# Kernel optimization log

Measured on AMD Instinct MI355X. Metric: run time of the kernel, lower is better.

The kernel has to match this reference:

```python
import jax, jax.numpy as jnp
import numpy as np

E = 1024   # embedding_dim
A = 1024   # attention_dim
H = 16     # num_heads
D = A // H # head_dim


def setup_inputs() -> dict:
    key = jax.random.key(0)
    ks = jax.random.split(key, 9)
    s = 1.0 / np.sqrt(E)
    so = 1.0 / np.sqrt(A)
    return {
        "x": jax.random.normal(ks[0], (2, 2048, E), dtype=jnp.float32),
        "Wq": jax.random.uniform(ks[1], (E, A), jnp.float32, -s, s),
        "bq": jax.random.uniform(ks[2], (A,), jnp.float32, -s, s),
        "Wk": jax.random.uniform(ks[3], (E, A), jnp.float32, -s, s),
        "bk": jax.random.uniform(ks[4], (A,), jnp.float32, -s, s),
        "Wv": jax.random.uniform(ks[5], (E, A), jnp.float32, -s, s),
        "bv": jax.random.uniform(ks[6], (A,), jnp.float32, -s, s),
        "Wo": jax.random.uniform(ks[7], (A, E), jnp.float32, -so, so),
        "bo": jax.random.uniform(ks[8], (E,), jnp.float32, -so, so),
    }


def reference(x, Wq, bq, Wk, bk, Wv, bv, Wo, bo):
    B, S, _ = x.shape
    # projections -> [B, H, S, D]
    def split_heads(t):
        return t.reshape(B, S, H, D).transpose(0, 2, 1, 3)
    Q = split_heads(x @ Wq + bq)
    K = split_heads(x @ Wk + bk)
    V = split_heads(x @ Wv + bv)
    scores = jnp.einsum("bhqd,bhkd->bhqk", Q, K) / jnp.sqrt(jnp.float32(D))
    causal = jnp.tril(jnp.ones((S, S), dtype=bool))
    scores = jnp.where(causal, scores, -jnp.inf)
    attn = jax.nn.softmax(scores, axis=-1)  # dropout p=0 (eval/deterministic)
    ctx = jnp.einsum("bhqk,bhkd->bhqd", attn, V)
    ctx = ctx.transpose(0, 2, 1, 3).reshape(B, S, A)
    out = ctx @ Wo + bo
    return (out, attn)
```

## Files before the change

kernel.cpp:

```cpp
#include <hip/hip_runtime.h>
#include <cstddef>

typedef __bf16 bf16_t;
typedef __attribute__((ext_vector_type(8))) __bf16 bf16x8;
typedef __attribute__((ext_vector_type(4))) float f32x4;

#define BATCH 2
#define SEQ   2048
#define EMB   1024
#define ADIM  1024
#define NHEAD 16
#define HDIM  64
#define MROWS 4096

__device__ inline unsigned short f2bf(float f) {
    bf16_t b = (bf16_t)f;
    return __builtin_bit_cast(unsigned short, b);
}

__global__ __launch_bounds__(256) void convert_x_kernel(
    const float* __restrict__ in, unsigned short* __restrict__ out, int n8)
{
    int i = blockIdx.x * 256 + threadIdx.x;
    if (i >= n8) return;
    const float4* p = (const float4*)(in + (size_t)i * 8);
    float4 a = p[0], b = p[1];
    unsigned int w0 = f2bf(a.x) | ((unsigned)f2bf(a.y) << 16);
    unsigned int w1 = f2bf(a.z) | ((unsigned)f2bf(a.w) << 16);
    unsigned int w2 = f2bf(b.x) | ((unsigned)f2bf(b.y) << 16);
    unsigned int w3 = f2bf(b.z) | ((unsigned)f2bf(b.w) << 16);
    uint4 v = {w0, w1, w2, w3};
    *(uint4*)(out + (size_t)i * 8) = v;
}

__global__ __launch_bounds__(256) void transpose_w_kernel(
    const float* __restrict__ Wq, const float* __restrict__ Wk,
    const float* __restrict__ Wv, const float* __restrict__ Wo,
    unsigned short* __restrict__ Wt_qkv, unsigned short* __restrict__ Wt_o)
{
    __shared__ float tile[64][65];
    const int m = blockIdx.z;
    const float* W = (m == 0) ? Wq : (m == 1) ? Wk : (m == 2) ? Wv : Wo;
    unsigned short* dst = (m < 3) ? (Wt_qkv + (size_t)m * 1024 * 1024) : Wt_o;
    const int r0 = blockIdx.y * 64, c0 = blockIdx.x * 64;
    const int t = threadIdx.x;
    const int r = t >> 2, c4 = (t & 3) * 16;
    #pragma unroll
    for (int j = 0; j < 16; j += 4) {
        float4 v = *(const float4*)(W + (size_t)(r0 + r) * 1024 + c0 + c4 + j);
        tile[r][c4 + j + 0] = v.x;
        tile[r][c4 + j + 1] = v.y;
        tile[r][c4 + j + 2] = v.z;
        tile[r][c4 + j + 3] = v.w;
    }
    __syncthreads();
    const int oc = t >> 2, ch = (t & 3) * 16;
    unsigned int ww[8];
    #pragma unroll
    for (int j = 0; j < 16; j += 2)
        ww[j >> 1] = f2bf(tile[ch + j][oc]) | ((unsigned)f2bf(tile[ch + j + 1][oc]) << 16);
    unsigned short* o = dst + (size_t)(c0 + oc) * 1024 + r0 + ch;
    *(uint4*)(o) = *(uint4*)&ww[0];
    *(uint4*)(o + 8) = *(uint4*)&ww[4];
}

template<int EPI>
__global__ __launch_bounds__(256) void gemm_mfma_kernel(
    const unsigned short* __restrict__ A,
    const unsigned short* __restrict__ Bt,
    const float* __restrict__ b0, const float* __restrict__ b1, const float* __restrict__ b2,
    void* __restrict__ outp, unsigned short* __restrict__ vt)
{
    __shared__ __align__(16) unsigned short Asm[4096];
    __shared__ __align__(16) unsigned short Bsm[4096];
    const int tid = threadIdx.x, lane = tid & 63, w = tid >> 6;
    const int wr = w >> 1, wc = w & 1;
    const int rowBase = blockIdx.y * 128, colBase = blockIdx.x * 128;
    const int K = 1024;

    f32x4 acc[4][4];
    #pragma unroll
    for (int i = 0; i < 4; ++i)
        #pragma unroll
        for (int j = 0; j < 4; ++j)
            acc[i][j] = (f32x4){0.f, 0.f, 0.f, 0.f};

    int mt_s[2], cc_s[2], r16_s[2];
    #pragma unroll
    for (int i = 0; i < 2; ++i) {
        int chunk = w * 128 + i * 64 + lane;
        mt_s[i] = chunk >> 6;
        cc_s[i] = (chunk & 63) >> 4;
        r16_s[i] = chunk & 15;
    }

    for (int k0 = 0; k0 < K; k0 += 32) {
        __syncthreads();
        #pragma unroll
        for (int i = 0; i < 2; ++i) {
            const unsigned short* ga = A + (size_t)(rowBase + mt_s[i] * 16 + r16_s[i]) * K + k0 + cc_s[i] * 8;
            __builtin_amdgcn_global_load_lds(
                (const __attribute__((address_space(1))) unsigned int*)ga,
                (__attribute__((address_space(3))) unsigned int*)(Asm + (size_t)(w * 128 + i * 64) * 8),
                16, 0, 0);
            const unsigned short* gb = Bt + (size_t)(colBase + mt_s[i] * 16 + r16_s[i]) * K + k0 + cc_s[i] * 8;
            __builtin_amdgcn_global_load_lds(
                (const __attribute__((address_space(1))) unsigned int*)gb,
                (__attribute__((address_space(3))) unsigned int*)(Bsm + (size_t)(w * 128 + i * 64) * 8),
                16, 0, 0);
        }
        __syncthreads();

        bf16x8 af[4], bfr[4];
        #pragma unroll
        for (int mt = 0; mt < 4; ++mt)
            af[mt] = *(const bf16x8*)(Asm + (size_t)((wr * 4 + mt) * 64 + lane) * 8);
        #pragma unroll
        for (int nt = 0; nt < 4; ++nt)
            bfr[nt] = *(const bf16x8*)(Bsm + (size_t)((wc * 4 + nt) * 64 + lane) * 8);
        #pragma unroll
        for (int mt = 0; mt < 4; ++mt)
            #pragma unroll
            for (int nt = 0; nt < 4; ++nt)
                acc[mt][nt] = __builtin_amdgcn_mfma_f32_16x16x32_bf16(af[mt], bfr[nt], acc[mt][nt], 0, 0, 0);
    }

    const int g = lane >> 4, r16 = lane & 15;
    const int seg = colBase >> 10;
    const float* bias = (seg == 0) ? b0 : (seg == 1) ? b1 : b2;

    if (EPI == 0) {
        unsigned short* qkv = (unsigned short*)outp;
        #pragma unroll
        for (int mt = 0; mt < 4; ++mt) {
            const int row0 = rowBase + wr * 64 + mt * 16 + 4 * g;
            #pragma unroll
            for (int nt = 0; nt < 4; ++nt) {
                const int col = colBase + wc * 64 + nt * 16 + r16;
                const float bb = bias[col & 1023];
                if (seg < 2) {
                    #pragma unroll
                    for (int rr = 0; rr < 4; ++rr)
                        qkv[(size_t)(row0 + rr) * 3072 + col] = f2bf(acc[mt][nt][rr] + bb);
                } else {
                    unsigned int p0 = f2bf(acc[mt][nt][0] + bb) | ((unsigned)f2bf(acc[mt][nt][1] + bb) << 16);
                    unsigned int p1 = f2bf(acc[mt][nt][2] + bb) | ((unsigned)f2bf(acc[mt][nt][3] + bb) << 16);
                    uint2 pv = {p0, p1};
                    *(uint2*)(vt + (size_t)(col - 2048) * 4096 + row0) = pv;
                }
            }
        }
    } else {
        float* out = (float*)outp;
        #pragma unroll
        for (int mt = 0; mt < 4; ++mt) {
            const int row0 = rowBase + wr * 64 + mt * 16 + 4 * g;
            #pragma unroll
            for (int nt = 0; nt < 4; ++nt) {
                const int col = colBase + wc * 64 + nt * 16 + r16;
                const float bb = bias[col];
                #pragma unroll
                for (int rr = 0; rr < 4; ++rr)
                    out[(size_t)(row0 + rr) * 1024 + col] = acc[mt][nt][rr] + bb;
            }
        }
    }
}

__global__ __launch_bounds__(256) void attn_mfma_kernel(
    const unsigned short* __restrict__ qkv,
    const unsigned short* __restrict__ vt,
    float* __restrict__ attn,
    unsigned short* __restrict__ ctx)
{
    __shared__ __align__(16) unsigned short Ksm[4096];
    __shared__ __align__(16) unsigned short Vsm[4096];
    __shared__ __align__(16) unsigned short Psm[4][1024];
    const int bh = blockIdx.x, b = bh >> 4, h = bh & 15;
    const int qt = 31 - (int)blockIdx.y;
    const int tid = threadIdx.x, lane = tid & 63, w = tid >> 6;
    const int g = lane >> 4, r16 = lane & 15;
    const int qrow0 = qt * 64 + w * 16;

    bf16x8 qf[2];
    #pragma unroll
    for (int k2 = 0; k2 < 2; ++k2)
        qf[k2] = *(const bf16x8*)(qkv + (size_t)(b * SEQ + qrow0 + r16) * 3072 + h * 64 + k2 * 32 + g * 8);

    const int sr = tid >> 2;
    const int sbc = (tid & 3) * 32;
    const int swz_s = (sr & 7) << 4;
    char* Kbase = (char*)Ksm;
    char* Vbase = (char*)Vsm;

    float rsum[4] = {0.f, 0.f, 0.f, 0.f};

    for (int kt = 0; kt <= qt; ++kt) {
        const int kbase = kt * 64;
        const char* gk = (const char*)(qkv + (size_t)(b * SEQ + kbase + sr) * 3072 + 1024 + h * 64);
        uint4 kv0 = *(const uint4*)(gk + sbc);
        uint4 kv1 = *(const uint4*)(gk + sbc + 16);
        __syncthreads();
        *(uint4*)(Kbase + ((sr * 128 + sbc) ^ swz_s)) = kv0;
        *(uint4*)(Kbase + ((sr * 128 + sbc + 16) ^ swz_s)) = kv1;
        __syncthreads();
        #pragma unroll
        for (int nt = 0; nt < 4; ++nt) {
            f32x4 s = {0.f, 0.f, 0.f, 0.f};
            const int krow = nt * 16 + r16;
            #pragma unroll
            for (int k2 = 0; k2 < 2; ++k2) {
                bf16x8 kf = *(const bf16x8*)(Kbase + ((krow * 128 + k2 * 64 + g * 16) ^ ((krow & 7) << 4)));
                s = __builtin_amdgcn_mfma_f32_16x16x32_bf16(qf[k2], kf, s, 0, 0, 0);
            }
            #pragma unroll
            for (int rr = 0; rr < 4; ++rr) {
                const int q = qrow0 + 4 * g + rr;
                const int k = kbase + nt * 16 + r16;
                if (k <= q) rsum[rr] += __expf(s[rr] * 0.125f);
            }
        }
    }
    #pragma unroll
    for (int rr = 0; rr < 4; ++rr) {
        float v = rsum[rr];
        v += __shfl_xor(v, 1, 64);
        v += __shfl_xor(v, 2, 64);
        v += __shfl_xor(v, 4, 64);
        v += __shfl_xor(v, 8, 64);
        rsum[rr] = 1.0f / v;
    }

    f32x4 cacc[4];
    #pragma unroll
    for (int nt = 0; nt < 4; ++nt) cacc[nt] = (f32x4){0.f, 0.f, 0.f, 0.f};

    for (int kt = 0; kt <= qt; ++kt) {
        const int kbase = kt * 64;
        const char* gk = (const char*)(qkv + (size_t)(b * SEQ + kbase + sr) * 3072 + 1024 + h * 64);
        uint4 kv0 = *(const uint4*)(gk + sbc);
        uint4 kv1 = *(const uint4*)(gk + sbc + 16);
        const char* gv = (const char*)(vt + (size_t)(h * 64 + sr) * 4096 + b * SEQ + kbase);
        uint4 vv0 = *(const uint4*)(gv + sbc);
        uint4 vv1 = *(const uint4*)(gv + sbc + 16);
        __syncthreads();
        *(uint4*)(Kbase + ((sr * 128 + sbc) ^ swz_s)) = kv0;
        *(uint4*)(Kbase + ((sr * 128 + sbc + 16) ^ swz_s)) = kv1;
        *(uint4*)(Vbase + ((sr * 128 + sbc) ^ swz_s)) = vv0;
        *(uint4*)(Vbase + ((sr * 128 + sbc + 16) ^ swz_s)) = vv1;
        __syncthreads();

        #pragma unroll
        for (int nt = 0; nt < 4; ++nt) {
            f32x4 s = {0.f, 0.f, 0.f, 0.f};
            const int krow = nt * 16 + r16;
            #pragma unroll
            for (int k2 = 0; k2 < 2; ++k2) {
                bf16x8 kf = *(const bf16x8*)(Kbase + ((krow * 128 + k2 * 64 + g * 16) ^ ((krow & 7) << 4)));
                s = __builtin_amdgcn_mfma_f32_16x16x32_bf16(qf[k2], kf, s, 0, 0, 0);
            }
            #pragma unroll
            for (int rr = 0; rr < 4; ++rr) {
                const int q = qrow0 + 4 * g + rr;
                const int k = kbase + nt * 16 + r16;
                float pn = 0.0f;
                if (k <= q) pn = __expf(s[rr] * 0.125f) * rsum[rr];
                attn[((size_t)bh * SEQ + q) * SEQ + k] = pn;
                const int prow = 4 * g + rr;
                *(unsigned short*)((char*)(Psm[w]) + ((prow * 128 + (nt * 16 + r16) * 2) ^ ((prow & 7) << 4))) = f2bf(pn);
            }
        }
        bf16x8 pf[2];
        #pragma unroll
        for (int k2 = 0; k2 < 2; ++k2)
            pf[k2] = *(const bf16x8*)((char*)(Psm[w]) + ((r16 * 128 + k2 * 64 + g * 16) ^ ((r16 & 7) << 4)));
        #pragma unroll
        for (int nt = 0; nt < 4; ++nt) {
            const int vrow = nt * 16 + r16;
            #pragma unroll
            for (int k2 = 0; k2 < 2; ++k2) {
                bf16x8 vf = *(const bf16x8*)(Vbase + ((vrow * 128 + k2 * 64 + g * 16) ^ ((vrow & 7) << 4)));
                cacc[nt] = __builtin_amdgcn_mfma_f32_16x16x32_bf16(pf[k2], vf, cacc[nt], 0, 0, 0);
            }
        }
    }

    #pragma unroll
    for (int nt = 0; nt < 4; ++nt)
        #pragma unroll
        for (int rr = 0; rr < 4; ++rr) {
            const int q = qrow0 + 4 * g + rr;
            ctx[(size_t)(b * SEQ + q) * 1024 + h * 64 + nt * 16 + r16] = f2bf(cacc[nt][rr]);
        }

    const int colStart = 64 * (qt + 1);
    const int Wc = SEQ - colStart;
    if (Wc > 0) {
        const int w4 = Wc >> 2;
        for (int c = tid; c < 64 * w4; c += 256) {
            const int row = qt * 64 + c / w4;
            const int col = colStart + (c % w4) * 4;
            *(float4*)(attn + ((size_t)bh * SEQ + row) * SEQ + col) = make_float4(0.f, 0.f, 0.f, 0.f);
        }
    }
}

extern "C" void kernel_launch(void* const* d_in, const int* in_sizes, int n_in,
                              void* d_out, int out_size, void* d_ws, size_t ws_size,
                              hipStream_t stream)
{
    const float* x  = (const float*)d_in[0];
    const float* Wq = (const float*)d_in[1];
    const float* bq = (const float*)d_in[2];
    const float* Wk = (const float*)d_in[3];
    const float* bk = (const float*)d_in[4];
    const float* Wv = (const float*)d_in[5];
    const float* bv = (const float*)d_in[6];
    const float* Wo = (const float*)d_in[7];
    const float* bo = (const float*)d_in[8];

    float* out  = (float*)d_out;
    float* attn = out + (size_t)BATCH * SEQ * EMB;

    unsigned short* xb     = (unsigned short*)d_ws;
    unsigned short* wt_qkv = xb + (size_t)MROWS * 1024;
    unsigned short* wt_o   = wt_qkv + (size_t)3072 * 1024;
    unsigned short* qkvb   = wt_o + (size_t)1024 * 1024;
    unsigned short* vtb    = qkvb + (size_t)MROWS * 3072;
    unsigned short* ctxb   = vtb + (size_t)1024 * MROWS;

    convert_x_kernel<<<2048, 256, 0, stream>>>(x, xb, MROWS * 1024 / 8);
    transpose_w_kernel<<<dim3(16, 16, 4), 256, 0, stream>>>(Wq, Wk, Wv, Wo, wt_qkv, wt_o);

    gemm_mfma_kernel<0><<<dim3(24, 32), 256, 0, stream>>>(xb, wt_qkv, bq, bk, bv, qkvb, vtb);

    attn_mfma_kernel<<<dim3(32, 32), 256, 0, stream>>>(qkvb, vtb, attn, ctxb);

    gemm_mfma_kernel<1><<<dim3(8, 32), 256, 0, stream>>>(ctxb, wt_o, bo, bo, bo, out, nullptr);
}
```

Baseline: 286.3 us.

## Double-buffer K/V tiles in attention and remap blocks across XCDs

Attention K and V tiles now use two shared-memory buffers. The next tile's global loads are issued before computing on the current tile and stored afterward, which leaves one barrier per iteration instead of two and hides load latency. The grid is flattened to 1D with a mapping that sends each head's blocks to the same XCD and interleaves query-tile lengths for load balance. Launch bounds request 4 blocks per CU. Shared memory per block grows, and the occupancy hint may constrain registers.

Result: faster. 255.6 us (-10.8%).

```diff
diff --git a/kernel.cpp b/kernel.cpp
--- a/kernel.cpp
+++ b/kernel.cpp
@@ -167,17 +167,22 @@
     }
 }
 
-__global__ __launch_bounds__(256) void attn_mfma_kernel(
+__global__ __launch_bounds__(256, 4) void attn_mfma_kernel(
     const unsigned short* __restrict__ qkv,
     const unsigned short* __restrict__ vt,
     float* __restrict__ attn,
     unsigned short* __restrict__ ctx)
 {
-    __shared__ __align__(16) unsigned short Ksm[4096];
-    __shared__ __align__(16) unsigned short Vsm[4096];
+    __shared__ __align__(16) unsigned short Ksm[2][4096];
+    __shared__ __align__(16) unsigned short Vsm[2][4096];
     __shared__ __align__(16) unsigned short Psm[4][1024];
-    const int bh = blockIdx.x, b = bh >> 4, h = bh & 15;
-    const int qt = 31 - (int)blockIdx.y;
+
+    const int j = blockIdx.x;
+    const int xcd = j & 7, slot = j >> 3;
+    const int bh = xcd + 8 * (slot & 3);
+    const int s4 = slot >> 2;
+    const int qt = 8 * (s4 >> 3) + (((s4 & 7) + 2 * (s4 >> 3)) & 7);
+    const int b = bh >> 4, h = bh & 15;
     const int tid = threadIdx.x, lane = tid & 63, w = tid >> 6;
     const int g = lane >> 4, r16 = lane & 15;
     const int qrow0 = qt * 64 + w * 16;
@@ -189,37 +194,51 @@
 
     const int sr = tid >> 2;
     const int sbc = (tid & 3) * 32;
-    const int swz_s = (sr & 7) << 4;
-    char* Kbase = (char*)Ksm;
-    char* Vbase = (char*)Vsm;
+    const int swz = (sr & 7) << 4;
+    char* Kb = (char*)Ksm;
+    char* Vb = (char*)Vsm;
 
     float rsum[4] = {0.f, 0.f, 0.f, 0.f};
 
+    {
+        const char* gk = (const char*)(qkv + (size_t)(b * SEQ + sr) * 3072 + 1024 + h * 64);
+        uint4 a0 = *(const uint4*)(gk + sbc);
+        uint4 a1 = *(const uint4*)(gk + sbc + 16);
+        *(uint4*)(Kb + ((sr * 128 + sbc) ^ swz)) = a0;
+        *(uint4*)(Kb + ((sr * 128 + sbc + 16) ^ swz)) = a1;
+    }
+    __syncthreads();
     for (int kt = 0; kt <= qt; ++kt) {
-        const int kbase = kt * 64;
-        const char* gk = (const char*)(qkv + (size_t)(b * SEQ + kbase + sr) * 3072 + 1024 + h * 64);
-        uint4 kv0 = *(const uint4*)(gk + sbc);
-        uint4 kv1 = *(const uint4*)(gk + sbc + 16);
-        __syncthreads();
-        *(uint4*)(Kbase + ((sr * 128 + sbc) ^ swz_s)) = kv0;
-        *(uint4*)(Kbase + ((sr * 128 + sbc + 16) ^ swz_s)) = kv1;
-        __syncthreads();
+        const int cur = kt & 1;
+        uint4 a0, a1;
+        if (kt < qt) {
+            const char* gk = (const char*)(qkv + (size_t)(b * SEQ + (kt + 1) * 64 + sr) * 3072 + 1024 + h * 64);
+            a0 = *(const uint4*)(gk + sbc);
+            a1 = *(const uint4*)(gk + sbc + 16);
+        }
+        const char* Kc = Kb + cur * 8192;
         #pragma unroll
         for (int nt = 0; nt < 4; ++nt) {
             f32x4 s = {0.f, 0.f, 0.f, 0.f};
             const int krow = nt * 16 + r16;
             #pragma unroll
             for (int k2 = 0; k2 < 2; ++k2) {
-                bf16x8 kf = *(const bf16x8*)(Kbase + ((krow * 128 + k2 * 64 + g * 16) ^ ((krow & 7) << 4)));
+                bf16x8 kf = *(const bf16x8*)(Kc + ((krow * 128 + k2 * 64 + g * 16) ^ ((krow & 7) << 4)));
                 s = __builtin_amdgcn_mfma_f32_16x16x32_bf16(qf[k2], kf, s, 0, 0, 0);
             }
             #pragma unroll
             for (int rr = 0; rr < 4; ++rr) {
                 const int q = qrow0 + 4 * g + rr;
-                const int k = kbase + nt * 16 + r16;
+                const int k = kt * 64 + nt * 16 + r16;
                 if (k <= q) rsum[rr] += __expf(s[rr] * 0.125f);
             }
         }
+        if (kt < qt) {
+            char* Kn = Kb + (cur ^ 1) * 8192;
+            *(uint4*)(Kn + ((sr * 128 + sbc) ^ swz)) = a0;
+            *(uint4*)(Kn + ((sr * 128 + sbc + 16) ^ swz)) = a1;
+        }
+        __syncthreads();
     }
     #pragma unroll
     for (int rr = 0; rr < 4; ++rr) {
@@ -235,20 +254,33 @@
     #pragma unroll
     for (int nt = 0; nt < 4; ++nt) cacc[nt] = (f32x4){0.f, 0.f, 0.f, 0.f};
 
+    {
+        const char* gk = (const char*)(qkv + (size_t)(b * SEQ + sr) * 3072 + 1024 + h * 64);
+        uint4 a0 = *(const uint4*)(gk + sbc);
+        uint4 a1 = *(const uint4*)(gk + sbc + 16);
+        const char* gv = (const char*)(vt + (size_t)(h * 64 + sr) * 4096 + b * SEQ);
+        uint4 v0 = *(const uint4*)(gv + sbc);
+        uint4 v1 = *(const uint4*)(gv + sbc + 16);
+        *(uint4*)(Kb + ((sr * 128 + sbc) ^ swz)) = a0;
+        *(uint4*)(Kb + ((sr * 128 + sbc + 16) ^ swz)) = a1;
+        *(uint4*)(Vb + ((sr * 128 + sbc) ^ swz)) = v0;
+        *(uint4*)(Vb + ((sr * 128 + sbc + 16) ^ swz)) = v1;
+    }
+    __syncthreads();
     for (int kt = 0; kt <= qt; ++kt) {
+        const int cur = kt & 1;
         const int kbase = kt * 64;
-        const char* gk = (const char*)(qkv + (size_t)(b * SEQ + kbase + sr) * 3072 + 1024 + h * 64);
-        uint4 kv0 = *(const uint4*)(gk + sbc);
-        uint4 kv1 = *(const uint4*)(gk + sbc + 16);
-        const char* gv = (const char*)(vt + (size_t)(h * 64 + sr) * 4096 + b * SEQ + kbase);
-        uint4 vv0 = *(const uint4*)(gv + sbc);
-        uint4 vv1 = *(const uint4*)(gv + sbc + 16);
-        __syncthreads();
-        *(uint4*)(Kbase + ((sr * 128 + sbc) ^ swz_s)) = kv0;
-        *(uint4*)(Kbase + ((sr * 128 + sbc + 16) ^ swz_s)) = kv1;
-        *(uint4*)(Vbase + ((sr * 128 + sbc) ^ swz_s)) = vv0;
-        *(uint4*)(Vbase + ((sr * 128 + sbc + 16) ^ swz_s)) = vv1;
-        __syncthreads();
+        uint4 a0, a1, v0, v1;
+        if (kt < qt) {
+            const char* gk = (const char*)(qkv + (size_t)(b * SEQ + kbase + 64 + sr) * 3072 + 1024 + h * 64);
+            a0 = *(const uint4*)(gk + sbc);
+            a1 = *(const uint4*)(gk + sbc + 16);
+            const char* gv = (const char*)(vt + (size_t)(h * 64 + sr) * 4096 + b * SEQ + kbase + 64);
+            v0 = *(const uint4*)(gv + sbc);
+            v1 = *(const uint4*)(gv + sbc + 16);
+        }
+        const char* Kc = Kb + cur * 8192;
+        const char* Vc = Vb + cur * 8192;
 
         #pragma unroll
         for (int nt = 0; nt < 4; ++nt) {
@@ -256,7 +288,7 @@
             const int krow = nt * 16 + r16;
             #pragma unroll
             for (int k2 = 0; k2 < 2; ++k2) {
-                bf16x8 kf = *(const bf16x8*)(Kbase + ((krow * 128 + k2 * 64 + g * 16) ^ ((krow & 7) << 4)));
+                bf16x8 kf = *(const bf16x8*)(Kc + ((krow * 128 + k2 * 64 + g * 16) ^ ((krow & 7) << 4)));
                 s = __builtin_amdgcn_mfma_f32_16x16x32_bf16(qf[k2], kf, s, 0, 0, 0);
             }
             #pragma unroll
@@ -279,10 +311,19 @@
             const int vrow = nt * 16 + r16;
             #pragma unroll
             for (int k2 = 0; k2 < 2; ++k2) {
-                bf16x8 vf = *(const bf16x8*)(Vbase + ((vrow * 128 + k2 * 64 + g * 16) ^ ((vrow & 7) << 4)));
+                bf16x8 vf = *(const bf16x8*)(Vc + ((vrow * 128 + k2 * 64 + g * 16) ^ ((vrow & 7) << 4)));
                 cacc[nt] = __builtin_amdgcn_mfma_f32_16x16x32_bf16(pf[k2], vf, cacc[nt], 0, 0, 0);
             }
         }
+        if (kt < qt) {
+            char* Kn = Kb + (cur ^ 1) * 8192;
+            char* Vn = Vb + (cur ^ 1) * 8192;
+            *(uint4*)(Kn + ((sr * 128 + sbc) ^ swz)) = a0;
+            *(uint4*)(Kn + ((sr * 128 + sbc + 16) ^ swz)) = a1;
+            *(uint4*)(Vn + ((sr * 128 + sbc) ^ swz)) = v0;
+            *(uint4*)(Vn + ((sr * 128 + sbc + 16) ^ swz)) = v1;
+        }
+        __syncthreads();
     }
 
     #pragma unroll
@@ -334,7 +375,7 @@
 
     gemm_mfma_kernel<0><<<dim3(24, 32), 256, 0, stream>>>(xb, wt_qkv, bq, bk, bv, qkvb, vtb);
 
-    attn_mfma_kernel<<<dim3(32, 32), 256, 0, stream>>>(qkvb, vtb, attn, ctxb);
+    attn_mfma_kernel<<<1024, 256, 0, stream>>>(qkvb, vtb, attn, ctxb);
 
     gemm_mfma_kernel<1><<<dim3(8, 32), 256, 0, stream>>>(ctxb, wt_o, bo, bo, bo, out, nullptr);
 }
```
